# Kernel optimization log

Hardware: AMD Instinct MI355X
Metric: run time of the kernel (lower is better)

Reference implementation:

```python
import jax, jax.numpy as jnp
import numpy as np

B, T, D_MODEL, N_HEADS = 2, 2048, 1024, 16
HEAD_DIM = D_MODEL // N_HEADS
GN_EPS = 1e-5


def decay_gammas(n_heads):
    # gamma_h = 1 - 2^(-5 - h*(8/n_heads))
    h = jnp.arange(n_heads, dtype=jnp.float32)
    return 1.0 - jnp.power(2.0, -5.0 - h * (8.0 / n_heads))


def setup_inputs() -> dict:
    key = jax.random.key(0)
    ks = jax.random.split(key, 7)
    w_scale = 0.02
    return {
        "x": jax.random.normal(ks[0], (B, T, D_MODEL), dtype=jnp.float32),
        "Wq": jax.random.normal(ks[1], (D_MODEL, D_MODEL), dtype=jnp.float32) * w_scale,
        "Wk": jax.random.normal(ks[2], (D_MODEL, D_MODEL), dtype=jnp.float32) * w_scale,
        "Wv": jax.random.normal(ks[3], (D_MODEL, D_MODEL), dtype=jnp.float32) * w_scale,
        "Wo": jax.random.normal(ks[4], (D_MODEL, D_MODEL), dtype=jnp.float32) * w_scale,
        "gn_w": jnp.ones((D_MODEL,), dtype=jnp.float32),
        "gn_b": jnp.zeros((D_MODEL,), dtype=jnp.float32),
    }


def reference(x, Wq, Wk, Wv, Wo, gn_w, gn_b):
    Bx, Tx, C = x.shape
    H, D = N_HEADS, C // N_HEADS
    gammas = decay_gammas(H)  # (H,)

    def split_heads(y):
        return y.reshape(Bx, Tx, H, D).transpose(0, 2, 1, 3)  # (B,H,T,D)

    # torch Linear: y = x @ W.T
    Q = split_heads(x @ Wq.T)
    K = split_heads(x @ Wk.T)
    V = split_heads(x @ Wv.T)

    # causal decay mask D[h,i,j] = gamma_h^(i-j) if i>=j else 0
    idx = jnp.arange(Tx, dtype=jnp.float32)
    diff = idx[:, None] - idx[None, :]  # (T,T)
    mask = jnp.where(diff >= 0,
                     gammas[:, None, None] ** jnp.maximum(diff, 0.0),
                     0.0)  # (H,T,T)

    scores = jnp.einsum("bhtd,bhsd->bhts", Q, K) / jnp.sqrt(jnp.float32(D))
    scores = scores * mask[None]  # (B,H,T,T)
    out = jnp.einsum("bhts,bhsd->bhtd", scores, V)  # (B,H,T,D)
    y = out.transpose(0, 2, 1, 3).reshape(Bx, Tx, C)  # merge heads

    # GroupNorm(n_heads, d_model) applied on (B, C, T): normalizes over
    # (head_dim, T) per group per batch element.
    z = y.transpose(0, 2, 1).reshape(Bx, H, D, Tx)
    mu = z.mean(axis=(2, 3), keepdims=True)
    var = z.var(axis=(2, 3), keepdims=True)
    zn = (z - mu) * jax.lax.rsqrt(var + GN_EPS)
    zn = zn * gn_w.reshape(1, H, D, 1) + gn_b.reshape(1, H, D, 1)
    y = zn.reshape(Bx, C, Tx).transpose(0, 2, 1)  # (B,T,C)

    return y @ Wo.T
```

## Files before the change

### kernel.cpp

```cpp
#include <hip/hip_runtime.h>
#include <hip/hip_bf16.h>

typedef __attribute__((ext_vector_type(8))) short short8;
typedef __attribute__((ext_vector_type(4))) float float4v;
typedef unsigned short u16;
typedef unsigned long long ull;

#define KD 1024

__device__ __forceinline__ u16 f2b(float f) {
    __hip_bfloat16 h = __float2bfloat16(f);
    return __builtin_bit_cast(u16, h);
}
__device__ __forceinline__ float b2f(u16 u) {
    unsigned x = ((unsigned)u) << 16;
    return __builtin_bit_cast(float, x);
}
__device__ __forceinline__ float lg_gamma(int h) {
    float gamma = 1.0f - exp2f(-5.0f - 0.5f * (float)h);
    return log2f(gamma);
}

__device__ __forceinline__ void async_cp16(const u16* g, u16* l) {
    __builtin_amdgcn_global_load_lds(
        (const __attribute__((address_space(1))) void*)g,
        (__attribute__((address_space(3))) void*)l,
        16, 0, 0);
}

__global__ __launch_bounds__(256)
void cvt_all(const float* __restrict__ x, const float* __restrict__ wq,
             const float* __restrict__ wk, const float* __restrict__ wv,
             const float* __restrict__ wo,
             u16* __restrict__ xb, u16* __restrict__ wqkvb, u16* __restrict__ wob)
{
    int bid = blockIdx.x;
    const float* src; u16* dst; long off; float sc = 1.0f;
    if (bid < 4096)      { src = x;  dst = xb;              off = (long)bid * 1024; }
    else if (bid < 5120) { src = wq; dst = wqkvb;           off = (long)(bid - 4096) * 1024; sc = 0.125f; }
    else if (bid < 6144) { src = wk; dst = wqkvb + 1048576; off = (long)(bid - 5120) * 1024; }
    else if (bid < 7168) { src = wv; dst = wqkvb + 2097152; off = (long)(bid - 6144) * 1024; }
    else                 { src = wo; dst = wob;             off = (long)(bid - 7168) * 1024; }
    long i = off + threadIdx.x * 4;
    float4 v = *(const float4*)(src + i);
    ushort4 u;
    u.x = f2b(v.x * sc); u.y = f2b(v.y * sc); u.z = f2b(v.z * sc); u.w = f2b(v.w * sc);
    *(ushort4*)(dst + i) = u;
}

template<int MODE>
__global__ __launch_bounds__(256)
void gemm_nt(const u16* __restrict__ A, const u16* __restrict__ Bw,
             u16* __restrict__ oQ, u16* __restrict__ oK,
             u16* __restrict__ oKt, u16* __restrict__ oVt,
             float* __restrict__ of)
{
    constexpr int TM = (MODE == 0) ? 128 : 64;
    constexpr int MI = (MODE == 0) ? 4 : 2;
    __shared__ __attribute__((aligned(16))) u16 Sh[(TM + 128) * 64];
    u16* As = Sh;
    u16* Bs = Sh + TM * 64;
    const int tid = threadIdx.x;
    const int lane = tid & 63;
    const int wv = tid >> 6;
    const int wm = wv >> 1, wn = wv & 1;
    const int row16 = lane & 15, quad = lane >> 4;
    const int lrow = lane >> 3, lseg = lane & 7;
    const int m0 = blockIdx.y * TM, n0 = blockIdx.x * 128;

    float4v acc[MI][4];
    float4v zero4 = {0.f, 0.f, 0.f, 0.f};
#pragma unroll
    for (int i = 0; i < MI; i++)
#pragma unroll
        for (int j = 0; j < 4; j++) acc[i][j] = zero4;

    const int scol = (lseg ^ lrow) << 3;

    for (int kt = 0; kt < KD; kt += 64) {
        __syncthreads();
#pragma unroll
        for (int i = 0; i < TM / 32; i++) {
            int r = wv * (TM / 4) + i * 8;
            async_cp16(A + (size_t)(m0 + r + lrow) * KD + kt + scol, &As[r * 64]);
        }
#pragma unroll
        for (int i = 0; i < 4; i++) {
            int r = wv * 32 + i * 8;
            async_cp16(Bw + (size_t)(n0 + r + lrow) * KD + kt + scol, &Bs[r * 64]);
        }
        __syncthreads();
#pragma unroll
        for (int kb = 0; kb < 2; kb++) {
            short8 af[MI], bf[4];
#pragma unroll
            for (int i = 0; i < MI; i++) {
                int row = wm * (MI * 16) + 16 * i + row16;
                af[i] = *(const short8*)(&As[row * 64 + (((kb * 4 + quad) ^ (row & 7)) << 3)]);
            }
#pragma unroll
            for (int j = 0; j < 4; j++) {
                int row = wn * 64 + 16 * j + row16;
                bf[j] = *(const short8*)(&Bs[row * 64 + (((kb * 4 + quad) ^ (row & 7)) << 3)]);
            }
#pragma unroll
            for (int i = 0; i < MI; i++)
#pragma unroll
                for (int j = 0; j < 4; j++)
                    acc[i][j] = __builtin_amdgcn_mfma_f32_16x16x32_bf16(af[i], bf[j], acc[i][j], 0, 0, 0);
        }
    }

    if (MODE == 0) {
        const int wsel = n0 >> 10;
        if (wsel <= 1) {
            u16* dst = (wsel == 0) ? oQ : oK;
#pragma unroll
            for (int i = 0; i < 4; i++)
#pragma unroll
                for (int j = 0; j < 4; j++) {
                    int gn = n0 + wn * 64 + 16 * j + row16;
                    int dd = gn & 63, hh = (gn >> 6) & 15;
#pragma unroll
                    for (int r = 0; r < 4; r++) {
                        int m = m0 + wm * 64 + 16 * i + quad * 4 + r;
                        int b = m >> 11, t = m & 2047;
                        dst[(size_t)(b * 16 + hh) * 131072 + t * 64 + dd] = f2b(acc[i][j][r]);
                    }
                }
        }
        if (wsel >= 1) {
            __syncthreads();
            u16* Tl = Sh + wv * 4096;
#pragma unroll
            for (int i = 0; i < 4; i++) {
                int m4 = 16 * i + quad * 4;
#pragma unroll
                for (int j = 0; j < 4; j++) {
                    int n_loc = 16 * j + row16;
                    ull pk = (ull)f2b(acc[i][j][0]) | ((ull)f2b(acc[i][j][1]) << 16) |
                             ((ull)f2b(acc[i][j][2]) << 32) | ((ull)f2b(acc[i][j][3]) << 48);
                    *(ull*)(&Tl[n_loc * 64 + (((m4 >> 3) ^ (n_loc & 7)) << 3) + (m4 & 7)]) = pk;
                }
            }
            __syncthreads();
            int gnb = n0 + wn * 64;
            int hh = (gnb >> 6) & 15;
            int mb = m0 + wm * 64;
            int bh = (mb >> 11) * 16 + hh;
            int t0 = mb & 2047;
            u16* dstT = (wsel == 1) ? oKt : oVt;
            int rr = lane >> 3, ss = lane & 7;
#pragma unroll
            for (int g = 0; g < 8; g++) {
                int row = 8 * g + rr;
                short8 v = *(const short8*)(&Tl[row * 64 + ((ss ^ rr) << 3)]);
                *(short8*)(&dstT[(size_t)bh * 131072 + (size_t)row * 2048 + t0 + ss * 8]) = v;
            }
        }
    } else {
#pragma unroll
        for (int i = 0; i < MI; i++)
#pragma unroll
            for (int j = 0; j < 4; j++) {
                int gn = n0 + wn * 64 + 16 * j + row16;
#pragma unroll
                for (int r = 0; r < 4; r++) {
                    int m = m0 + wm * 32 + 16 * i + quad * 4 + r;
                    of[(size_t)m * 1024 + gn] = acc[i][j][r];
                }
            }
    }
}

__global__ __launch_bounds__(256)
void chunk_state(const u16* __restrict__ Kt, const u16* __restrict__ Vt,
                 float* __restrict__ U)
{
    const int c = blockIdx.x, bh = blockIdx.y, h = bh & 15;
    const int tid = threadIdx.x, lane = tid & 63, w = tid >> 6;
    const int row16 = lane & 15, quad = lane >> 4;
    const float lg = lg_gamma(h);
    const size_t base = (size_t)bh * 131072;

    float4v acc[4];
    float4v zero4 = {0.f, 0.f, 0.f, 0.f};
#pragma unroll
    for (int tn = 0; tn < 4; tn++) acc[tn] = zero4;

#pragma unroll
    for (int kb = 0; kb < 2; kb++) {
        short8 a = *(const short8*)(Vt + base + (size_t)(16 * w + row16) * 2048 + c * 64 + kb * 32 + quad * 8);
        short8 as;
        int e0 = 63 - (kb * 32 + quad * 8);
#pragma unroll
        for (int jj = 0; jj < 8; jj++) {
            float v = b2f((u16)a[jj]) * exp2f(lg * (float)(e0 - jj));
            as[jj] = (short)f2b(v);
        }
#pragma unroll
        for (int tn = 0; tn < 4; tn++) {
            short8 bfr = *(const short8*)(Kt + base + (size_t)(16 * tn + row16) * 2048 + c * 64 + kb * 32 + quad * 8);
            acc[tn] = __builtin_amdgcn_mfma_f32_16x16x32_bf16(as, bfr, acc[tn], 0, 0, 0);
        }
    }
    float* up = U + ((size_t)bh * 32 + c) * 4096;
#pragma unroll
    for (int tn = 0; tn < 4; tn++)
#pragma unroll
        for (int r = 0; r < 4; r++)
            up[(16 * w + quad * 4 + r) * 64 + 16 * tn + row16] = acc[tn][r];
}

__global__ __launch_bounds__(256)
void state_scan(const float* __restrict__ U, u16* __restrict__ St)
{
    const int bh = blockIdx.y;
    const int e = blockIdx.x * 256 + threadIdx.x;
    const float g64 = exp2f(lg_gamma(bh & 15) * 64.0f);
    float s = 0.f;
    St[(size_t)bh * 131072 + e] = 0;
    for (int c = 1; c < 32; c++) {
        s = g64 * s + U[((size_t)bh * 32 + (c - 1)) * 4096 + e];
        St[((size_t)bh * 32 + c) * 4096 + e] = f2b(s);
    }
}

__global__ __launch_bounds__(256)
void retention_chunk(const u16* __restrict__ Q, const u16* __restrict__ Kb,
                     const u16* __restrict__ Vt, const u16* __restrict__ St,
                     float* __restrict__ Y, float* __restrict__ stats)
{
    __shared__ __attribute__((aligned(16))) u16 Pl[4][16 * 72];
    __shared__ float red[8];
    const int c = blockIdx.x, bh = blockIdx.y, h = bh & 15;
    const int tid = threadIdx.x, lane = tid & 63, w = tid >> 6;
    const int row16 = lane & 15, quad = lane >> 4;
    const float lg = lg_gamma(h);
    const size_t base = (size_t)bh * 131072;
    float4v zero4 = {0.f, 0.f, 0.f, 0.f};

    short8 qf[2];
#pragma unroll
    for (int kb = 0; kb < 2; kb++)
        qf[kb] = *(const short8*)(Q + base + (size_t)(c * 64 + 16 * w + row16) * 64 + kb * 32 + quad * 8);

    float4v accp[4];
#pragma unroll
    for (int tn = 0; tn < 4; tn++) accp[tn] = zero4;
#pragma unroll
    for (int tn = 0; tn < 4; tn++)
#pragma unroll
        for (int kb = 0; kb < 2; kb++) {
            short8 kf = *(const short8*)(Kb + base + (size_t)(c * 64 + 16 * tn + row16) * 64 + kb * 32 + quad * 8);
            accp[tn] = __builtin_amdgcn_mfma_f32_16x16x32_bf16(qf[kb], kf, accp[tn], 0, 0, 0);
        }
#pragma unroll
    for (int tn = 0; tn < 4; tn++)
#pragma unroll
        for (int r = 0; r < 4; r++) {
            int a_loc = 16 * w + quad * 4 + r;
            int b_loc = 16 * tn + row16;
            int d = a_loc - b_loc;
            float v = (d >= 0) ? accp[tn][r] * exp2f(lg * (float)d) : 0.f;
            Pl[w][(quad * 4 + r) * 72 + b_loc] = f2b(v);
        }
    __syncthreads();

    short8 pf[2];
#pragma unroll
    for (int kb = 0; kb < 2; kb++)
        pf[kb] = *(const short8*)(&Pl[w][row16 * 72 + kb * 32 + quad * 8]);

    float4v acco[4], acci[4];
#pragma unroll
    for (int tn = 0; tn < 4; tn++) { acco[tn] = zero4; acci[tn] = zero4; }
#pragma unroll
    for (int tn = 0; tn < 4; tn++)
#pragma unroll
        for (int kb = 0; kb < 2; kb++) {
            short8 vf = *(const short8*)(Vt + base + (size_t)(16 * tn + row16) * 2048 + c * 64 + kb * 32 + quad * 8);
            acco[tn] = __builtin_amdgcn_mfma_f32_16x16x32_bf16(pf[kb], vf, acco[tn], 0, 0, 0);
            short8 sf = *(const short8*)(St + ((size_t)bh * 32 + c) * 4096 + (16 * tn + row16) * 64 + kb * 32 + quad * 8);
            acci[tn] = __builtin_amdgcn_mfma_f32_16x16x32_bf16(qf[kb], sf, acci[tn], 0, 0, 0);
        }

    float s = 0.f, s2 = 0.f;
#pragma unroll
    for (int tn = 0; tn < 4; tn++)
#pragma unroll
        for (int r = 0; r < 4; r++) {
            int a_loc = 16 * w + quad * 4 + r;
            float gi = exp2f(lg * (float)(a_loc + 1));
            int t = c * 64 + a_loc, d2 = 16 * tn + row16;
            float yv = acco[tn][r] + gi * acci[tn][r];
            Y[(size_t)bh * 131072 + t * 64 + d2] = yv;
            s += yv;
            s2 += yv * yv;
        }
#pragma unroll
    for (int off = 32; off; off >>= 1) {
        s += __shfl_down(s, off, 64);
        s2 += __shfl_down(s2, off, 64);
    }
    if (lane == 0) { red[w] = s; red[4 + w] = s2; }
    __syncthreads();
    if (tid == 0) {
        atomicAdd(&stats[2 * bh], red[0] + red[1] + red[2] + red[3]);
        atomicAdd(&stats[2 * bh + 1], red[4] + red[5] + red[6] + red[7]);
    }
}

__global__ __launch_bounds__(256)
void gn_apply(const float* __restrict__ Y, const float* __restrict__ stats,
              const float* __restrict__ gnw, const float* __restrict__ gnb,
              u16* __restrict__ Z)
{
    int i4 = (blockIdx.x * 256 + threadIdx.x) * 4;
    int b = i4 >> 21, t = (i4 >> 10) & 2047, cc = i4 & 1023;
    int hh = cc >> 6, dd = cc & 63, bh = b * 16 + hh;
    float4 v = *(const float4*)(Y + (size_t)bh * 131072 + t * 64 + dd);
    float S = stats[2 * bh], S2 = stats[2 * bh + 1];
    float mu = S * (1.0f / 131072.f);
    float var = S2 * (1.0f / 131072.f) - mu * mu;
    float rsg = rsqrtf(var + 1e-5f);
    float4 wv = *(const float4*)(gnw + cc);
    float4 bv = *(const float4*)(gnb + cc);
    ushort4 o;
    o.x = f2b((v.x - mu) * rsg * wv.x + bv.x);
    o.y = f2b((v.y - mu) * rsg * wv.y + bv.y);
    o.z = f2b((v.z - mu) * rsg * wv.z + bv.z);
    o.w = f2b((v.w - mu) * rsg * wv.w + bv.w);
    *(ushort4*)(Z + i4) = o;
}

extern "C" void kernel_launch(void* const* d_in, const int* in_sizes, int n_in,
                              void* d_out, int out_size, void* d_ws, size_t ws_size,
                              hipStream_t stream) {
    const float* x   = (const float*)d_in[0];
    const float* Wq  = (const float*)d_in[1];
    const float* Wk  = (const float*)d_in[2];
    const float* Wv  = (const float*)d_in[3];
    const float* Wo  = (const float*)d_in[4];
    const float* gnw = (const float*)d_in[5];
    const float* gnb = (const float*)d_in[6];
    float* out = (float*)d_out;
    char* ws = (char*)d_ws;

    u16*  xb    = (u16*)(ws + 0);
    u16*  wqkvb = (u16*)(ws + 8388608);
    u16*  wob   = (u16*)(ws + 14680064);
    u16*  Qs    = (u16*)(ws + 16777216);
    u16*  Kb    = (u16*)(ws + 25165824);
    u16*  Kt    = (u16*)(ws + 33554432);
    u16*  Vt    = (u16*)(ws + 41943040);
    float* U    = (float*)(ws + 50331648);
    u16*  St    = (u16*)(ws + 67108864);
    float* Y    = (float*)(ws + 75497472);
    u16*  Zb    = (u16*)(ws + 92274688);
    float* stats= (float*)(ws + 100663296);

    hipMemsetAsync(stats, 0, 64 * sizeof(float), stream);

    cvt_all<<<8192, 256, 0, stream>>>(x, Wq, Wk, Wv, Wo, xb, wqkvb, wob);

    gemm_nt<0><<<dim3(24, 32), 256, 0, stream>>>(xb, wqkvb, Qs, Kb, Kt, Vt, nullptr);

    chunk_state<<<dim3(32, 32), 256, 0, stream>>>(Kt, Vt, U);
    state_scan<<<dim3(16, 32), 256, 0, stream>>>(U, St);
    retention_chunk<<<dim3(32, 32), 256, 0, stream>>>(Qs, Kb, Vt, St, Y, stats);

    gn_apply<<<4096, 256, 0, stream>>>(Y, stats, gnw, gnb, Zb);

    gemm_nt<1><<<dim3(8, 64), 256, 0, stream>>>(Zb, wob, nullptr, nullptr, nullptr, nullptr, out);
}
```

Baseline: 196.0 us.

## Switch GEMMs to 32x32x16 MFMA and store chunk states in bf16

The projection GEMMs now use 32x32x16 bf16 MFMA instructions in place of 16x16x32, with fragment loads and epilogue index mapping rewritten for the 32x32 accumulator layout. The aim is fewer LDS fragment loads per MFMA and higher matrix-core throughput. Separately, the per-chunk state buffer U is written and read as bf16 instead of fp32, halving that intermediate's memory traffic. The bf16 U adds rounding error to the state scan accumulation.

```diff
diff --git a/kernel.cpp b/kernel.cpp
--- a/kernel.cpp
+++ b/kernel.cpp
@@ -3,6 +3,7 @@
 
 typedef __attribute__((ext_vector_type(8))) short short8;
 typedef __attribute__((ext_vector_type(4))) float float4v;
+typedef __attribute__((ext_vector_type(16))) float float16v;
 typedef unsigned short u16;
 typedef unsigned long long ull;
 
@@ -56,7 +57,7 @@
              float* __restrict__ of)
 {
     constexpr int TM = (MODE == 0) ? 128 : 64;
-    constexpr int MI = (MODE == 0) ? 4 : 2;
+    constexpr int MI = (MODE == 0) ? 2 : 1;
     __shared__ __attribute__((aligned(16))) u16 Sh[(TM + 128) * 64];
     u16* As = Sh;
     u16* Bs = Sh + TM * 64;
@@ -64,16 +65,17 @@
     const int lane = tid & 63;
     const int wv = tid >> 6;
     const int wm = wv >> 1, wn = wv & 1;
-    const int row16 = lane & 15, quad = lane >> 4;
+    const int row32 = lane & 31, khalf = lane >> 5;
     const int lrow = lane >> 3, lseg = lane & 7;
     const int m0 = blockIdx.y * TM, n0 = blockIdx.x * 128;
 
-    float4v acc[MI][4];
-    float4v zero4 = {0.f, 0.f, 0.f, 0.f};
+    float16v acc[MI][2];
 #pragma unroll
     for (int i = 0; i < MI; i++)
 #pragma unroll
-        for (int j = 0; j < 4; j++) acc[i][j] = zero4;
+        for (int j = 0; j < 2; j++)
+#pragma unroll
+            for (int r = 0; r < 16; r++) acc[i][j][r] = 0.f;
 
     const int scol = (lseg ^ lrow) << 3;
 
@@ -91,23 +93,23 @@
         }
         __syncthreads();
 #pragma unroll
-        for (int kb = 0; kb < 2; kb++) {
-            short8 af[MI], bf[4];
+        for (int ks = 0; ks < 4; ks++) {
+            short8 af[MI], bf[2];
 #pragma unroll
             for (int i = 0; i < MI; i++) {
-                int row = wm * (MI * 16) + 16 * i + row16;
-                af[i] = *(const short8*)(&As[row * 64 + (((kb * 4 + quad) ^ (row & 7)) << 3)]);
+                int row = wm * (MI * 32) + i * 32 + row32;
+                af[i] = *(const short8*)(&As[row * 64 + (((ks * 2 + khalf) ^ (row & 7)) << 3)]);
             }
 #pragma unroll
-            for (int j = 0; j < 4; j++) {
-                int row = wn * 64 + 16 * j + row16;
-                bf[j] = *(const short8*)(&Bs[row * 64 + (((kb * 4 + quad) ^ (row & 7)) << 3)]);
+            for (int j = 0; j < 2; j++) {
+                int row = wn * 64 + j * 32 + row32;
+                bf[j] = *(const short8*)(&Bs[row * 64 + (((ks * 2 + khalf) ^ (row & 7)) << 3)]);
             }
 #pragma unroll
             for (int i = 0; i < MI; i++)
 #pragma unroll
-                for (int j = 0; j < 4; j++)
-                    acc[i][j] = __builtin_amdgcn_mfma_f32_16x16x32_bf16(af[i], bf[j], acc[i][j], 0, 0, 0);
+                for (int j = 0; j < 2; j++)
+                    acc[i][j] = __builtin_amdgcn_mfma_f32_32x32x16_bf16(af[i], bf[j], acc[i][j], 0, 0, 0);
         }
     }
 
@@ -116,16 +118,16 @@
         if (wsel <= 1) {
             u16* dst = (wsel == 0) ? oQ : oK;
 #pragma unroll
-            for (int i = 0; i < 4; i++)
-#pragma unroll
-                for (int j = 0; j < 4; j++) {
-                    int gn = n0 + wn * 64 + 16 * j + row16;
+            for (int i = 0; i < 2; i++)
+#pragma unroll
+                for (int j = 0; j < 2; j++) {
+                    int gn = n0 + wn * 64 + j * 32 + row32;
                     int dd = gn & 63, hh = (gn >> 6) & 15;
 #pragma unroll
-                    for (int r = 0; r < 4; r++) {
-                        int m = m0 + wm * 64 + 16 * i + quad * 4 + r;
+                    for (int reg = 0; reg < 16; reg++) {
+                        int m = m0 + wm * 64 + i * 32 + (reg & 3) + 8 * (reg >> 2) + 4 * khalf;
                         int b = m >> 11, t = m & 2047;
-                        dst[(size_t)(b * 16 + hh) * 131072 + t * 64 + dd] = f2b(acc[i][j][r]);
+                        dst[(size_t)(b * 16 + hh) * 131072 + t * 64 + dd] = f2b(acc[i][j][reg]);
                     }
                 }
         }
@@ -133,16 +135,18 @@
             __syncthreads();
             u16* Tl = Sh + wv * 4096;
 #pragma unroll
-            for (int i = 0; i < 4; i++) {
-                int m4 = 16 * i + quad * 4;
-#pragma unroll
-                for (int j = 0; j < 4; j++) {
-                    int n_loc = 16 * j + row16;
-                    ull pk = (ull)f2b(acc[i][j][0]) | ((ull)f2b(acc[i][j][1]) << 16) |
-                             ((ull)f2b(acc[i][j][2]) << 32) | ((ull)f2b(acc[i][j][3]) << 48);
-                    *(ull*)(&Tl[n_loc * 64 + (((m4 >> 3) ^ (n_loc & 7)) << 3) + (m4 & 7)]) = pk;
+            for (int i = 0; i < 2; i++)
+#pragma unroll
+                for (int j = 0; j < 2; j++) {
+                    int n_loc = j * 32 + row32;
+#pragma unroll
+                    for (int g = 0; g < 4; g++) {
+                        int m4 = i * 32 + 8 * g + 4 * khalf;
+                        ull pk = (ull)f2b(acc[i][j][4 * g]) | ((ull)f2b(acc[i][j][4 * g + 1]) << 16) |
+                                 ((ull)f2b(acc[i][j][4 * g + 2]) << 32) | ((ull)f2b(acc[i][j][4 * g + 3]) << 48);
+                        *(ull*)(&Tl[n_loc * 64 + (((m4 >> 3) ^ (n_loc & 7)) << 3) + (m4 & 7)]) = pk;
+                    }
                 }
-            }
             __syncthreads();
             int gnb = n0 + wn * 64;
             int hh = (gnb >> 6) & 15;
@@ -160,22 +164,20 @@
         }
     } else {
 #pragma unroll
-        for (int i = 0; i < MI; i++)
-#pragma unroll
-            for (int j = 0; j < 4; j++) {
-                int gn = n0 + wn * 64 + 16 * j + row16;
-#pragma unroll
-                for (int r = 0; r < 4; r++) {
-                    int m = m0 + wm * 32 + 16 * i + quad * 4 + r;
-                    of[(size_t)m * 1024 + gn] = acc[i][j][r];
-                }
+        for (int j = 0; j < 2; j++) {
+            int gn = n0 + wn * 64 + j * 32 + row32;
+#pragma unroll
+            for (int reg = 0; reg < 16; reg++) {
+                int m = m0 + wm * 32 + (reg & 3) + 8 * (reg >> 2) + 4 * khalf;
+                of[(size_t)m * 1024 + gn] = acc[0][j][reg];
             }
+        }
     }
 }
 
 __global__ __launch_bounds__(256)
 void chunk_state(const u16* __restrict__ Kt, const u16* __restrict__ Vt,
-                 float* __restrict__ U)
+                 u16* __restrict__ U)
 {
     const int c = blockIdx.x, bh = blockIdx.y, h = bh & 15;
     const int tid = threadIdx.x, lane = tid & 63, w = tid >> 6;
@@ -204,16 +206,16 @@
             acc[tn] = __builtin_amdgcn_mfma_f32_16x16x32_bf16(as, bfr, acc[tn], 0, 0, 0);
         }
     }
-    float* up = U + ((size_t)bh * 32 + c) * 4096;
+    u16* up = U + ((size_t)bh * 32 + c) * 4096;
 #pragma unroll
     for (int tn = 0; tn < 4; tn++)
 #pragma unroll
         for (int r = 0; r < 4; r++)
-            up[(16 * w + quad * 4 + r) * 64 + 16 * tn + row16] = acc[tn][r];
-}
-
-__global__ __launch_bounds__(256)
-void state_scan(const float* __restrict__ U, u16* __restrict__ St)
+            up[(16 * w + quad * 4 + r) * 64 + 16 * tn + row16] = f2b(acc[tn][r]);
+}
+
+__global__ __launch_bounds__(256)
+void state_scan(const u16* __restrict__ U, u16* __restrict__ St)
 {
     const int bh = blockIdx.y;
     const int e = blockIdx.x * 256 + threadIdx.x;
@@ -221,7 +223,7 @@
     float s = 0.f;
     St[(size_t)bh * 131072 + e] = 0;
     for (int c = 1; c < 32; c++) {
-        s = g64 * s + U[((size_t)bh * 32 + (c - 1)) * 4096 + e];
+        s = g64 * s + b2f(U[((size_t)bh * 32 + (c - 1)) * 4096 + e]);
         St[((size_t)bh * 32 + c) * 4096 + e] = f2b(s);
     }
 }
@@ -354,7 +356,7 @@
     u16*  Kb    = (u16*)(ws + 25165824);
     u16*  Kt    = (u16*)(ws + 33554432);
     u16*  Vt    = (u16*)(ws + 41943040);
-    float* U    = (float*)(ws + 50331648);
+    u16*  U     = (u16*)(ws + 50331648);
     u16*  St    = (u16*)(ws + 67108864);
     float* Y    = (float*)(ws + 75497472);
     u16*  Zb    = (u16*)(ws + 92274688);
```

New measurement: 188.4 us. 1.04x faster.
